# Optimization experiments

Measured on AMD Instinct MI355X. Metric: run time of the kernel, lower is better.

Reference implementation:

```python
import jax, jax.numpy as jnp
import numpy as np

EPS = 1.1920929e-07  # torch RMSNorm default eps = finfo(fp32).eps
NUM_HEADS = 8
UP_HEAD = 64
ROPE_HEAD = 32
TOP_K = 4
HIDDEN = 512
INTER = 256
DQ = 256
DKV = 128
N_EXPERTS = 16
B, S = 2, 2048


def _rmsnorm(x, w):
    return x * jax.lax.rsqrt(jnp.mean(x * x, axis=-1, keepdims=True) + EPS) * w


def _rope(x):
    # x: [B, h, S, D] with D = ROPE_HEAD; rotate-half RoPE, base 10000
    D = x.shape[-1]
    s = x.shape[-2]
    inv_freq = 1.0 / (10000.0 ** (jnp.arange(0, D, 2, dtype=jnp.float32) / D))
    freqs = jnp.outer(jnp.arange(s, dtype=jnp.float32), inv_freq)  # [S, D/2]
    emb = jnp.concatenate([freqs, freqs], axis=-1)  # [S, D]
    cos, sin = jnp.cos(emb), jnp.sin(emb)
    x1, x2 = x[..., : D // 2], x[..., D // 2:]
    rot = jnp.concatenate([-x2, x1], axis=-1)
    return x * cos + rot * sin


def _swiglu(x, wg, wu, wd):
    return (jax.nn.silu(x @ wg) * (x @ wu)) @ wd


def setup_inputs() -> dict:
    key = jax.random.key(0)
    ks = jax.random.split(key, 18)
    sd = 0.02
    inp = {
        "hidden_states": jax.random.normal(ks[0], (B, S, HIDDEN), jnp.float32),
        "w_in_norm": jnp.ones((HIDDEN,), jnp.float32),
        "w_dq": sd * jax.random.normal(ks[1], (HIDDEN, DQ), jnp.float32),
        "w_qnorm": jnp.ones((DQ,), jnp.float32),
        "w_uq": sd * jax.random.normal(ks[2], (DQ, NUM_HEADS * (UP_HEAD + ROPE_HEAD)), jnp.float32),
        "w_dkv": sd * jax.random.normal(ks[3], (HIDDEN, DKV + ROPE_HEAD), jnp.float32),
        "w_kvnorm": jnp.ones((DKV,), jnp.float32),
        "w_ukv": sd * jax.random.normal(ks[4], (DKV, NUM_HEADS * UP_HEAD * 2), jnp.float32),
        "w_o": sd * jax.random.normal(ks[5], (NUM_HEADS * UP_HEAD, HIDDEN), jnp.float32),
        "w_post_norm": jnp.ones((HIDDEN,), jnp.float32),
        "w_gate": sd * jax.random.normal(ks[6], (HIDDEN, N_EXPERTS), jnp.float32),
        "sh_wg": sd * jax.random.normal(ks[7], (HIDDEN, INTER), jnp.float32),
        "sh_wu": sd * jax.random.normal(ks[8], (HIDDEN, INTER), jnp.float32),
        "sh_wd": sd * jax.random.normal(ks[9], (INTER, HIDDEN), jnp.float32),
        "r_wg": sd * jax.random.normal(ks[10], (N_EXPERTS, HIDDEN, INTER), jnp.float32),
        "r_wu": sd * jax.random.normal(ks[11], (N_EXPERTS, HIDDEN, INTER), jnp.float32),
        "r_wd": sd * jax.random.normal(ks[12], (N_EXPERTS, INTER, HIDDEN), jnp.float32),
    }
    return inp


def reference(hidden_states, w_in_norm, w_dq, w_qnorm, w_uq, w_dkv, w_kvnorm,
              w_ukv, w_o, w_post_norm, w_gate, sh_wg, sh_wu, sh_wd,
              r_wg, r_wu, r_wd):
    b, s, h = hidden_states.shape
    # ---- MLA attention block ----
    residual = hidden_states
    x = _rmsnorm(hidden_states, w_in_norm)
    c_q = x @ w_dq                                             # [B,S,Dq]
    qcr = _rmsnorm(c_q, w_qnorm) @ w_uq                        # [B,S,nh*(uh+rh)]
    qcr = qcr.reshape(b, s, NUM_HEADS, UP_HEAD + ROPE_HEAD).transpose(0, 2, 1, 3)
    q_c, q_r = qcr[..., :UP_HEAD], qcr[..., UP_HEAD:]
    ckv_kr = x @ w_dkv                                         # [B,S,Dkv+rh]
    c_kv, k_r = ckv_kr[..., :DKV], ckv_kr[..., DKV:]
    k_r = k_r[:, None, :, :]                                   # [B,1,S,rh]
    kv = (_rmsnorm(c_kv, w_kvnorm) @ w_ukv).reshape(b, s, NUM_HEADS, 2 * UP_HEAD).transpose(0, 2, 1, 3)
    k_c, v = kv[..., :UP_HEAD], kv[..., UP_HEAD:]
    q = jnp.concatenate([q_c, _rope(q_r)], axis=-1)            # [B,nh,S,96]
    k = jnp.concatenate([k_c, jnp.broadcast_to(_rope(k_r), (b, NUM_HEADS, s, ROPE_HEAD))], axis=-1)
    scale = 1.0 / jnp.sqrt(jnp.float32(UP_HEAD + ROPE_HEAD))
    attn = jax.nn.softmax(jnp.einsum('bhqd,bhkd->bhqk', q, k) * scale, axis=-1)
    o = jnp.einsum('bhqk,bhkd->bhqd', attn, v).transpose(0, 2, 1, 3).reshape(b, s, NUM_HEADS * UP_HEAD)
    x = o @ w_o + residual
    # ---- MoE block ----
    residual = x
    x = _rmsnorm(x, w_post_norm)
    x2 = x.reshape(-1, h)                                      # [T,H]
    shared = _swiglu(x2, sh_wg, sh_wu, sh_wd)                  # [T,H]
    scores = jax.nn.sigmoid(x2 @ w_gate)                       # [T,E]
    tw, ti = jax.lax.top_k(scores, TOP_K)                      # [T,k]
    tw = tw / jnp.sum(tw, axis=-1, keepdims=True)
    # combine[t,e] = routing weight of expert e for token t (0 if not selected)
    combine = jnp.sum(jax.nn.one_hot(ti, N_EXPERTS, dtype=x2.dtype) * tw[..., None], axis=1)  # [T,E]
    g = jnp.einsum('th,ehi->tei', x2, r_wg)
    u = jnp.einsum('th,ehi->tei', x2, r_wu)
    y = jnp.einsum('tei,eih->teh', jax.nn.silu(g) * u, r_wd)   # per-expert SwiGLU outputs
    routed = jnp.einsum('teh,te->th', y, combine)
    return (shared + routed).reshape(b, s, h) + residual
```

## Files before the change

kernel.cpp:

```cpp
#include <hip/hip_runtime.h>
#include <hip/hip_bf16.h>
#include <math.h>

typedef float f32x4 __attribute__((ext_vector_type(4)));
typedef short s16x8 __attribute__((ext_vector_type(8)));

constexpr int Tt = 4096;
constexpr int NEn = 16;
constexpr float EPSf = 1.1920929e-07f;

__device__ __forceinline__ short f2b(float f) {
    union { __hip_bfloat16 h; short s; } u;
    u.h = __float2bfloat16(f);
    return u.s;
}
__device__ __forceinline__ float b2f(short s) {
    union { float f; unsigned u; } v;
    v.u = ((unsigned)(unsigned short)s) << 16;
    return v.f;
}

constexpr size_t alg(size_t x) { return (x + 15) & ~(size_t)15; }
constexpr size_t OFF_CQKV = 0;
constexpr size_t OFF_QCR  = alg(OFF_CQKV + (size_t)Tt * 416);
constexpr size_t OFF_KVB  = alg(OFF_QCR  + (size_t)Tt * 768);
constexpr size_t OFF_R2   = alg(OFF_KVB  + (size_t)Tt * 1024);
constexpr size_t OFF_TOKE = alg(OFF_R2   + (size_t)Tt * 512);
constexpr size_t OFF_TOKW = alg(OFF_TOKE + (size_t)Tt * 4);
constexpr size_t OFF_EWT  = alg(OFF_TOKW + (size_t)Tt * 4);
constexpr size_t OFF_ECNT = alg(OFF_EWT  + (size_t)NEn * Tt);
constexpr size_t OFF_ETOK = alg(OFF_ECNT + 64);
constexpr size_t OFF_PO   = 0;
constexpr size_t OFF_PL   = (size_t)16 * 2048 * 4 * 64 / 2;
constexpr size_t OFF_XNB   = alg(OFF_ETOK + (size_t)NEn * Tt);
constexpr size_t OFF_CQNB  = alg(OFF_XNB   + (size_t)Tt * 512 / 2);
constexpr size_t OFF_CKVNB = alg(OFF_CQNB  + (size_t)Tt * 256 / 2);
constexpr size_t OFF_QB    = alg(OFF_CKVNB + (size_t)Tt * 128 / 2);
constexpr size_t OFF_KB    = alg(OFF_QB    + (size_t)16 * 2048 * 96 / 2);
constexpr size_t OFF_VBT   = alg(OFF_KB    + (size_t)16 * 2048 * 96 / 2);
constexpr size_t OFF_XN2B  = alg(OFF_VBT   + (size_t)16 * 64 * 2048 / 2);
constexpr size_t OFF_GACT  = alg(OFF_XN2B  + (size_t)Tt * 512 / 2);
constexpr size_t OFF_EACT  = alg(OFF_GACT  + (size_t)Tt * 256 / 2);
constexpr size_t OFF_WQKVT = alg(OFF_EACT  + (size_t)16384 * 256 / 2);
constexpr size_t OFF_WUQT  = alg(OFF_WQKVT + (size_t)416 * 512 / 2);
constexpr size_t OFF_WUKVT = alg(OFF_WUQT  + (size_t)768 * 256 / 2);
constexpr size_t OFF_WOT   = alg(OFF_WUKVT + (size_t)1024 * 128 / 2);
constexpr size_t OFF_SHWGT = alg(OFF_WOT   + (size_t)512 * 512 / 2);
constexpr size_t OFF_SHWUT = alg(OFF_SHWGT + (size_t)256 * 512 / 2);
constexpr size_t OFF_SHWDT = alg(OFF_SHWUT + (size_t)256 * 512 / 2);
constexpr size_t OFF_RWGT  = alg(OFF_SHWDT + (size_t)512 * 256 / 2);
constexpr size_t OFF_RWUT  = alg(OFF_RWGT  + (size_t)16 * 256 * 512 / 2);
constexpr size_t OFF_RWDT  = alg(OFF_RWUT  + (size_t)16 * 256 * 512 / 2);

struct CvtTab {
    const float* src[11];
    short* dst[11];
    int K[11], N[11], end[11];
};
__global__ __launch_bounds__(256)
void k_cvt_all(CvtTab tab) {
    __shared__ float t[32][33];
    int bid = blockIdx.x;
    int i = 0;
    while (bid >= tab.end[i]) ++i;
    int tloc = bid - (i ? tab.end[i - 1] : 0);
    int K = tab.K[i], N = tab.N[i];
    int ntiles = N >> 5, perE = ntiles * (K >> 5);
    int e = tloc / perE, rem = tloc - e * perE;
    int k0 = (rem / ntiles) << 5, n0 = (rem % ntiles) << 5;
    size_t eo = (size_t)e * K * N;
    const float* src = tab.src[i];
    short* dst = tab.dst[i];
    int c = threadIdx.x & 31, r = threadIdx.x >> 5;
#pragma unroll
    for (int q = 0; q < 4; ++q)
        t[r + 8 * q][c] = src[eo + (size_t)(k0 + r + 8 * q) * N + n0 + c];
    __syncthreads();
#pragma unroll
    for (int q = 0; q < 4; ++q)
        dst[eo + (size_t)(n0 + r + 8 * q) * K + k0 + c] = f2b(t[c][r + 8 * q]);
}

__global__ void k_rms(const float* __restrict__ in, int inStride, const float* __restrict__ w,
                      short* __restrict__ outB, int outStride, int D) {
    int row = blockIdx.x, tid = threadIdx.x;
    __shared__ float xs[512];
    __shared__ float red[256];
    const float* ip = in + (size_t)row * inStride;
    float ss = 0.f;
    for (int i = tid; i < D; i += 256) { float v = ip[i]; xs[i] = v; ss += v * v; }
    red[tid] = ss; __syncthreads();
    for (int s = 128; s > 0; s >>= 1) { if (tid < s) red[tid] += red[tid + s]; __syncthreads(); }
    float sc = rsqrtf(red[0] / (float)D + EPSf);
    for (int i = tid; i < D; i += 256) outB[(size_t)row * outStride + i] = f2b(xs[i] * sc * w[i]);
}

__global__ void k_rms2(const float* __restrict__ cqkv, const float* __restrict__ wq, short* __restrict__ cqnb,
                       const float* __restrict__ wkv, short* __restrict__ ckvnb) {
    int row = blockIdx.x, tid = threadIdx.x;
    __shared__ float xs[256];
    __shared__ float red[256];
    const float* ip; const float* w; short* ob; int D, outStride, r;
    if (row < Tt) { r = row;      ip = cqkv + (size_t)r * 416;       w = wq;  ob = cqnb;  D = 256; outStride = 256; }
    else          { r = row - Tt; ip = cqkv + (size_t)r * 416 + 256; w = wkv; ob = ckvnb; D = 128; outStride = 128; }
    float ss = 0.f;
    for (int i = tid; i < D; i += 256) { float v = ip[i]; xs[i] = v; ss += v * v; }
    red[tid] = ss; __syncthreads();
    for (int s = 128; s > 0; s >>= 1) { if (tid < s) red[tid] += red[tid + s]; __syncthreads(); }
    float sc = rsqrtf(red[0] / (float)D + EPSf);
    for (int i = tid; i < D; i += 256) ob[(size_t)r * outStride + i] = f2b(xs[i] * sc * w[i]);
}

__global__ __launch_bounds__(256)
void k_rms_router(const float* __restrict__ r2, const float* __restrict__ wpost,
                  const float* __restrict__ wg,
                  short* __restrict__ xn2b, int4* __restrict__ toke, float4* __restrict__ tokw) {
    int t = blockIdx.x, tid = threadIdx.x;
    __shared__ float xs[512];
    __shared__ float red[256];
    __shared__ float part[16][17];
    __shared__ float sc[16];
    const float* ip = r2 + (size_t)t * 512;
    float ss = 0.f;
    for (int i = tid; i < 512; i += 256) { float v = ip[i]; xs[i] = v; ss += v * v; }
    red[tid] = ss; __syncthreads();
    for (int s = 128; s > 0; s >>= 1) { if (tid < s) red[tid] += red[tid + s]; __syncthreads(); }
    float scale = rsqrtf(red[0] / 512.f + EPSf);
    for (int i = tid; i < 512; i += 256) {
        float v = xs[i] * scale * wpost[i];
        xs[i] = v;
        xn2b[(size_t)t * 512 + i] = f2b(v);
    }
    __syncthreads();
    {
        int e = tid & 15, ch = tid >> 4;
        const float* wp = wg + (size_t)ch * 32 * 16 + e;
        float s = 0.f;
#pragma unroll 8
        for (int k = 0; k < 32; ++k) s = fmaf(xs[ch * 32 + k], wp[(size_t)k * 16], s);
        part[ch][e] = s;
    }
    __syncthreads();
    if (tid < 16) {
        float s = 0.f;
#pragma unroll
        for (int c = 0; c < 16; ++c) s += part[c][tid];
        sc[tid] = 1.f / (1.f + expf(-s));
    }
    __syncthreads();
    if (tid < 64) {
        int lane = tid, e = lane & 15;
        float scv = sc[e];
        unsigned sel = 0;
        float tw[4]; int ti[4];
#pragma unroll
        for (int kk = 0; kk < 4; ++kk) {
            float cand = ((sel >> e) & 1u) ? -1e30f : scv;
            float mx = cand;
            mx = fmaxf(mx, __shfl_xor(mx, 1));
            mx = fmaxf(mx, __shfl_xor(mx, 2));
            mx = fmaxf(mx, __shfl_xor(mx, 4));
            mx = fmaxf(mx, __shfl_xor(mx, 8));
            unsigned long long msk = __ballot(cand == mx);
            int bi = (__ffsll(msk) - 1) & 15;
            tw[kk] = mx; ti[kk] = bi;
            sel |= 1u << bi;
        }
        if (lane == 0) {
            float inv = 1.f / (tw[0] + tw[1] + tw[2] + tw[3]);
            toke[t] = make_int4(ti[0], ti[1], ti[2], ti[3]);
            tokw[t] = make_float4(tw[0] * inv, tw[1] * inv, tw[2] * inv, tw[3] * inv);
        }
    }
}

template <int EPI>
__global__ __launch_bounds__(512)
void k_mgemm(const short* __restrict__ A, const short* __restrict__ BT,
             void* __restrict__ Cv, const float* __restrict__ add, int N, int K) {
    __shared__ __align__(16) short As[64 * 64];
    __shared__ __align__(16) short Bs[64 * 64];
    int tid = threadIdx.x;
    int w = tid >> 6, l = tid & 63, g = l >> 4, li = l & 15;
    int wm = w >> 1, wn = w & 1;
    int m0 = blockIdx.y * 64, n0 = blockIdx.x * 64;
    f32x4 acc[2] = {};
    for (int k0 = 0; k0 < K; k0 += 64) {
        __syncthreads();
        {
            int row = tid >> 3, ch = tid & 7;
            *(int4*)&As[row * 64 + ((ch ^ (row & 7)) * 8)] =
                *(const int4*)(A + (size_t)(m0 + row) * K + k0 + 8 * ch);
            int4 v = {0, 0, 0, 0};
            if (n0 + row < N) v = *(const int4*)(BT + (size_t)(n0 + row) * K + k0 + 8 * ch);
            *(int4*)&Bs[row * 64 + ((ch ^ (row & 7)) * 8)] = v;
        }
        __syncthreads();
#pragma unroll
        for (int kc = 0; kc < 2; ++kc) {
            int row = wm * 16 + li;
            s16x8 af = *(const s16x8*)&As[row * 64 + (((4 * kc + g) ^ (li & 7)) * 8)];
#pragma unroll
            for (int nt = 0; nt < 2; ++nt) {
                int n = wn * 32 + nt * 16 + li;
                s16x8 bf = *(const s16x8*)&Bs[n * 64 + (((4 * kc + g) ^ (li & 7)) * 8)];
                acc[nt] = __builtin_amdgcn_mfma_f32_16x16x32_bf16(af, bf, acc[nt], 0, 0, 0);
            }
        }
    }
#pragma unroll
    for (int nt = 0; nt < 2; ++nt)
#pragma unroll
        for (int r = 0; r < 4; ++r) {
            int gm = m0 + wm * 16 + 4 * g + r;
            int gn = n0 + wn * 32 + nt * 16 + li;
            if (gn < N) {
                float v = acc[nt][r];
                if (EPI == 1) v += add[(size_t)gm * N + gn];
                if (EPI == 2) ((short*)Cv)[(size_t)gm * N + gn] = f2b(v);
                else          ((float*)Cv)[(size_t)gm * N + gn] = v;
            }
        }
}

__global__ __launch_bounds__(512)
void k_wo_gemm(const short* __restrict__ po, const float* __restrict__ pl,
               const short* __restrict__ BT, float* __restrict__ C,
               const float* __restrict__ add) {
    constexpr int N = 512, K = 512;
    __shared__ __align__(16) short As[64 * 64];
    __shared__ __align__(16) short Bs[64 * 64];
    int tid = threadIdx.x;
    int w = tid >> 6, l = tid & 63, g = l >> 4, li = l & 15;
    int wm = w >> 1, wn = w & 1;
    int m0 = blockIdx.y * 64, n0 = blockIdx.x * 64;
    int row = tid >> 3, ch = tid & 7;
    int t = m0 + row;
    int b = t >> 11, q = t & 2047;
    f32x4 acc[2] = {};
    for (int k0 = 0; k0 < K; k0 += 64) {
        int h = k0 >> 6;
        int bhq = (b * 8 + h) * 2048 + q;
        size_t pb = (size_t)bhq * 256 + 8 * ch;
        float4 l4 = *(const float4*)(pl + (size_t)bhq * 4);
        float inv = 1.f / (l4.x + l4.y + l4.z + l4.w);
        union { int4 v; short s[8]; } p0, p1, p2, p3, ov;
        p0.v = *(const int4*)(po + pb);
        p1.v = *(const int4*)(po + pb + 64);
        p2.v = *(const int4*)(po + pb + 128);
        p3.v = *(const int4*)(po + pb + 192);
#pragma unroll
        for (int i = 0; i < 8; ++i) {
            float os = b2f(p0.s[i]) + b2f(p1.s[i]) + b2f(p2.s[i]) + b2f(p3.s[i]);
            ov.s[i] = f2b(os * inv);
        }
        int4 bv = *(const int4*)(BT + (size_t)(n0 + row) * K + k0 + 8 * ch);
        __syncthreads();
        *(int4*)&As[row * 64 + ((ch ^ (row & 7)) * 8)] = ov.v;
        *(int4*)&Bs[row * 64 + ((ch ^ (row & 7)) * 8)] = bv;
        __syncthreads();
#pragma unroll
        for (int kc = 0; kc < 2; ++kc) {
            int rr = wm * 16 + li;
            s16x8 af = *(const s16x8*)&As[rr * 64 + (((4 * kc + g) ^ (li & 7)) * 8)];
#pragma unroll
            for (int nt = 0; nt < 2; ++nt) {
                int n = wn * 32 + nt * 16 + li;
                s16x8 bf = *(const s16x8*)&Bs[n * 64 + (((4 * kc + g) ^ (li & 7)) * 8)];
                acc[nt] = __builtin_amdgcn_mfma_f32_16x16x32_bf16(af, bf, acc[nt], 0, 0, 0);
            }
        }
    }
#pragma unroll
    for (int nt = 0; nt < 2; ++nt)
#pragma unroll
        for (int r = 0; r < 4; ++r) {
            int gm = m0 + wm * 16 + 4 * g + r;
            int gn = n0 + wn * 32 + nt * 16 + li;
            C[(size_t)gm * N + gn] = acc[nt][r] + add[(size_t)gm * N + gn];
        }
}

__global__ __launch_bounds__(512)
void k_shexp(const short* __restrict__ X, const short* __restrict__ WGt, const short* __restrict__ WUt,
             short* __restrict__ gact) {
    __shared__ __align__(16) short As[64 * 64];
    __shared__ __align__(16) short Bg[64 * 64];
    __shared__ __align__(16) short Bu[64 * 64];
    int tid = threadIdx.x;
    int w = tid >> 6, l = tid & 63, g = l >> 4, li = l & 15;
    int wm = w >> 1, wn = w & 1;
    int m0 = blockIdx.x * 64, n0 = blockIdx.y * 64;
    f32x4 ag[2] = {}, au[2] = {};
    for (int k0 = 0; k0 < 512; k0 += 64) {
        __syncthreads();
        {
            int row = tid >> 3, ch = tid & 7;
            *(int4*)&As[row * 64 + ((ch ^ (row & 7)) * 8)] =
                *(const int4*)(X + (size_t)(m0 + row) * 512 + k0 + 8 * ch);
            *(int4*)&Bg[row * 64 + ((ch ^ (row & 7)) * 8)] =
                *(const int4*)(WGt + (size_t)(n0 + row) * 512 + k0 + 8 * ch);
            *(int4*)&Bu[row * 64 + ((ch ^ (row & 7)) * 8)] =
                *(const int4*)(WUt + (size_t)(n0 + row) * 512 + k0 + 8 * ch);
        }
        __syncthreads();
#pragma unroll
        for (int kc = 0; kc < 2; ++kc) {
            int row = wm * 16 + li;
            s16x8 af = *(const s16x8*)&As[row * 64 + (((4 * kc + g) ^ (li & 7)) * 8)];
#pragma unroll
            for (int nt = 0; nt < 2; ++nt) {
                int n = wn * 32 + nt * 16 + li;
                s16x8 bg = *(const s16x8*)&Bg[n * 64 + (((4 * kc + g) ^ (li & 7)) * 8)];
                s16x8 bu = *(const s16x8*)&Bu[n * 64 + (((4 * kc + g) ^ (li & 7)) * 8)];
                ag[nt] = __builtin_amdgcn_mfma_f32_16x16x32_bf16(af, bg, ag[nt], 0, 0, 0);
                au[nt] = __builtin_amdgcn_mfma_f32_16x16x32_bf16(af, bu, au[nt], 0, 0, 0);
            }
        }
    }
#pragma unroll
    for (int nt = 0; nt < 2; ++nt)
#pragma unroll
        for (int r = 0; r < 4; ++r) {
            int gm = m0 + wm * 16 + 4 * g + r;
            int gn = n0 + wn * 32 + nt * 16 + li;
            float gv = ag[nt][r], uv = au[nt][r];
            gact[(size_t)gm * 256 + gn] = f2b(gv / (1.f + __expf(-gv)) * uv);
        }
}

__global__ void k_build_qkv(const short* __restrict__ qcrb, const short* __restrict__ kvbb,
                            const float* __restrict__ cqkv,
                            short* __restrict__ qb, short* __restrict__ kb, short* __restrict__ vbt) {
    const float scale = 0.14724389f;
    int gid = blockIdx.x * 256 + threadIdx.x;
    const int NQ = 16 * 2048 * 96;
    if (gid < NQ) {
        int d = gid % 96;
        int rs = gid / 96;
        int srow = rs & 2047;
        int bh = rs >> 11;
        int b = bh >> 3, h = bh & 7;
        int t = b * 2048 + srow;
        const short* src = qcrb + (size_t)t * 768 + h * 96;
        float val;
        if (d < 64) {
            val = b2f(src[d]);
        } else {
            int d2 = d - 64;
            int fi = d2 & 15;
            float ang = (float)srow * __expf(-((float)(2 * fi) / 32.f) * 9.210340371976184f);
            float s, c; __sincosf(ang, &s, &c);
            float x = b2f(src[64 + d2]);
            float r = (d2 < 16) ? -b2f(src[64 + d2 + 16]) : b2f(src[64 + d2 - 16]);
            val = x * c + r * s;
        }
        qb[gid] = f2b(val * scale);
    } else if (gid < 2 * NQ) {
        int g2 = gid - NQ;
        int d = g2 % 96;
        int rs = g2 / 96;
        int srow = rs & 2047;
        int bh = rs >> 11;
        int b = bh >> 3, h = bh & 7;
        int t = b * 2048 + srow;
        if (d < 64) {
            kb[g2] = kvbb[(size_t)t * 1024 + h * 128 + d];
        } else {
            int d2 = d - 64;
            int fi = d2 & 15;
            float ang = (float)srow * __expf(-((float)(2 * fi) / 32.f) * 9.210340371976184f);
            float s, c; __sincosf(ang, &s, &c);
            float x = cqkv[(size_t)t * 416 + 384 + d2];
            float r = (d2 < 16) ? -cqkv[(size_t)t * 416 + 384 + d2 + 16]
                                :  cqkv[(size_t)t * 416 + 384 + d2 - 16];
            kb[g2] = f2b(x * c + r * s);
        }
    } else {
        int g2 = gid - 2 * NQ;
        int key = g2 & 2047;
        int dim = (g2 >> 11) & 63;
        int bh = g2 >> 17;
        int b = bh >> 3, h = bh & 7;
        vbt[g2] = kvbb[(size_t)(b * 2048 + key) * 1024 + h * 128 + 64 + dim];
    }
}

__global__ __launch_bounds__(256)
void k_attn(const short* __restrict__ qb, const short* __restrict__ kb,
            const short* __restrict__ vbt, short* __restrict__ po, float* __restrict__ pl) {
    __shared__ __align__(16) short Ks[64 * 100];
    __shared__ __align__(16) short Vs[80 * 64];
    int tid = threadIdx.x;
    int w = tid >> 6, l = tid & 63, g = l >> 4, li = l & 15;
    int blk = blockIdx.x;
    int bh = blk >> 6, rem = blk & 63;
    int qt = rem >> 2, ks = rem & 3;
    int qc0 = qt * 128 + w * 32;

    {
        const short one = 0x3F80;
        for (int i = tid; i < 16 * 64; i += 256)
            Vs[64 * 64 + i] = (i < 64) ? one : (short)0;
    }

    s16x8 qf[2][3];
#pragma unroll
    for (int j = 0; j < 2; ++j) {
        const short* qp = qb + (size_t)(bh * 2048 + qc0 + j * 16 + li) * 96;
#pragma unroll
        for (int c = 0; c < 3; ++c) qf[j][c] = *(const s16x8*)(qp + 32 * c + 8 * g);
    }

    f32x4 o[2][5] = {};
    const short* kbase = kb + (size_t)bh * 2048 * 96;
    const short* vbase = vbt + (size_t)bh * 64 * 2048;

    for (int t = 0; t < 8; ++t) {
        int koff = ks * 512 + t * 64;
        __syncthreads();
#pragma unroll
        for (int p = 0; p < 3; ++p) {
            int flat = p * 256 + tid;
            int key = flat / 12, u = flat % 12;
            *(int4*)&Ks[key * 100 + 8 * u] = *(const int4*)(kbase + (size_t)(koff + key) * 96 + 8 * u);
        }
#pragma unroll
        for (int p = 0; p < 2; ++p) {
            int flat = p * 256 + tid;
            int dim = flat >> 3, kc8 = flat & 7;
            int4 v = *(const int4*)(vbase + (size_t)dim * 2048 + koff + 8 * kc8);
            int sw = dim & 15;
            *(int2*)&Vs[dim * 64 + (((2 * kc8) ^ sw) * 4)]     = make_int2(v.x, v.y);
            *(int2*)&Vs[dim * 64 + (((2 * kc8 + 1) ^ sw) * 4)] = make_int2(v.z, v.w);
        }
        __syncthreads();

        f32x4 s[2][4];
#pragma unroll
        for (int kt = 0; kt < 4; ++kt) {
            f32x4 a0 = {}, a1 = {};
#pragma unroll
            for (int c = 0; c < 3; ++c) {
                s16x8 kf = *(const s16x8*)&Ks[(kt * 16 + li) * 100 + 32 * c + 8 * g];
                a0 = __builtin_amdgcn_mfma_f32_16x16x32_bf16(kf, qf[0][c], a0, 0, 0, 0);
                a1 = __builtin_amdgcn_mfma_f32_16x16x32_bf16(kf, qf[1][c], a1, 0, 0, 0);
            }
            s[0][kt] = a0; s[1][kt] = a1;
        }
#pragma unroll
        for (int j = 0; j < 2; ++j)
#pragma unroll
            for (int kt = 0; kt < 4; ++kt)
#pragma unroll
                for (int r = 0; r < 4; ++r) s[j][kt][r] = exp2f(s[j][kt][r]);
        s16x8 pf[2][2];
#pragma unroll
        for (int j = 0; j < 2; ++j)
#pragma unroll
            for (int kc = 0; kc < 2; ++kc) {
                s16x8 tt;
#pragma unroll
                for (int r = 0; r < 4; ++r) { tt[r] = f2b(s[j][2 * kc][r]); tt[4 + r] = f2b(s[j][2 * kc + 1][r]); }
                pf[j][kc] = tt;
            }
#pragma unroll
        for (int dt = 0; dt < 5; ++dt) {
            int dim = dt * 16 + li;
#pragma unroll
            for (int kc = 0; kc < 2; ++kc) {
                int2 a0 = *(const int2*)&Vs[dim * 64 + (((8 * kc + g) ^ li) * 4)];
                int2 a1 = *(const int2*)&Vs[dim * 64 + (((8 * kc + 4 + g) ^ li) * 4)];
                union { s16x8 v; int i[4]; } vf;
                vf.i[0] = a0.x; vf.i[1] = a0.y; vf.i[2] = a1.x; vf.i[3] = a1.y;
                o[0][dt] = __builtin_amdgcn_mfma_f32_16x16x32_bf16(vf.v, pf[0][kc], o[0][dt], 0, 0, 0);
                o[1][dt] = __builtin_amdgcn_mfma_f32_16x16x32_bf16(vf.v, pf[1][kc], o[1][dt], 0, 0, 0);
            }
        }
    }
#pragma unroll
    for (int j = 0; j < 2; ++j) {
        int qcol = qc0 + j * 16 + li;
        size_t qbase = ((size_t)(bh * 2048 + qcol) * 4 + ks) * 64;
#pragma unroll
        for (int dt = 0; dt < 4; ++dt)
#pragma unroll
            for (int r = 0; r < 4; ++r)
                po[qbase + dt * 16 + 4 * g + r] = f2b(o[j][dt][r]);
        if (g == 0) pl[(size_t)(bh * 2048 + qcol) * 4 + ks] = o[j][4][0];
    }
}

__global__ __launch_bounds__(256)
void k_scatter(const int4* __restrict__ toke, const float4* __restrict__ tokw,
               float* __restrict__ ewt, int* __restrict__ ecnt, int* __restrict__ etok) {
    __shared__ int lcnt[16];
    __shared__ int lbase[16];
    int tid = threadIdx.x;
    int t = blockIdx.x * 256 + tid;
    if (tid < 16) lcnt[tid] = 0;
    __syncthreads();
    int4 e4 = toke[t];
    float4 w4 = tokw[t];
    int es[4] = { e4.x, e4.y, e4.z, e4.w };
    float wv[4] = { w4.x, w4.y, w4.z, w4.w };
    int ls[4];
#pragma unroll
    for (int kk = 0; kk < 4; ++kk) ls[kk] = atomicAdd(&lcnt[es[kk]], 1);
    __syncthreads();
    if (tid < 16) lbase[tid] = atomicAdd(&ecnt[tid], lcnt[tid]);
    __syncthreads();
#pragma unroll
    for (int kk = 0; kk < 4; ++kk) {
        int slot = lbase[es[kk]] + ls[kk];
        etok[es[kk] * 4096 + slot] = t * 4 + kk;
        ewt[es[kk] * 4096 + slot] = wv[kk];
    }
}

__global__ __launch_bounds__(512)
void k_moe1m(const short* __restrict__ X, const short* __restrict__ WGt, const short* __restrict__ WUt,
             const int* __restrict__ ecnt, const int* __restrict__ etok, short* __restrict__ eact) {
    __shared__ int ecs[16];
    __shared__ __align__(16) short As[128 * 64];
    __shared__ __align__(16) short Bg[64 * 64];
    __shared__ __align__(16) short Bu[64 * 64];
    __shared__ int toks[128];
    int tid = threadIdx.x;
    if (tid < 16) ecs[tid] = ecnt[tid];
    __syncthreads();
    int bid = blockIdx.x, e = 0;
    for (; e < 16; ++e) { int n = (ecs[e] + 127) >> 7; if (bid < n) break; bid -= n; }
    if (e >= 16) return;
    int base = bid << 7;
    int rows = min(128, ecs[e] - base);
    int n0 = blockIdx.y * 64;
    if (tid < 128) toks[tid] = (tid < rows) ? etok[e * 4096 + base + tid] : -1;
    __syncthreads();
    int w = tid >> 6, l = tid & 63, g = l >> 4, li = l & 15;
    int wm = w >> 1, wn = w & 1;
    const short* wgp = WGt + (size_t)e * 256 * 512;
    const short* wup = WUt + (size_t)e * 256 * 512;
    f32x4 ag[2][2] = {}, au[2][2] = {};
    for (int k0 = 0; k0 < 512; k0 += 64) {
        __syncthreads();
#pragma unroll
        for (int p = 0; p < 2; ++p) {
            int flat = p * 512 + tid;
            int row = flat >> 3, ch = flat & 7;
            int tk = toks[row];
            int4 v = {0, 0, 0, 0};
            if (tk >= 0) v = *(const int4*)(X + (size_t)(tk >> 2) * 512 + k0 + 8 * ch);
            *(int4*)&As[row * 64 + ((ch ^ (row & 7)) * 8)] = v;
        }
        {
            int n = tid >> 3, ch = tid & 7;
            *(int4*)&Bg[n * 64 + ((ch ^ (n & 7)) * 8)] = *(const int4*)(wgp + (size_t)(n0 + n) * 512 + k0 + 8 * ch);
            *(int4*)&Bu[n * 64 + ((ch ^ (n & 7)) * 8)] = *(const int4*)(wup + (size_t)(n0 + n) * 512 + k0 + 8 * ch);
        }
        __syncthreads();
#pragma unroll
        for (int kc = 0; kc < 2; ++kc) {
            s16x8 af[2], bg[2], bu[2];
#pragma unroll
            for (int mt = 0; mt < 2; ++mt) {
                int row = wm * 32 + mt * 16 + li;
                af[mt] = *(const s16x8*)&As[row * 64 + (((4 * kc + g) ^ (li & 7)) * 8)];
            }
#pragma unroll
            for (int nt = 0; nt < 2; ++nt) {
                int n = wn * 32 + nt * 16 + li;
                bg[nt] = *(const s16x8*)&Bg[n * 64 + (((4 * kc + g) ^ (li & 7)) * 8)];
                bu[nt] = *(const s16x8*)&Bu[n * 64 + (((4 * kc + g) ^ (li & 7)) * 8)];
            }
#pragma unroll
            for (int mt = 0; mt < 2; ++mt)
#pragma unroll
                for (int nt = 0; nt < 2; ++nt) {
                    ag[mt][nt] = __builtin_amdgcn_mfma_f32_16x16x32_bf16(af[mt], bg[nt], ag[mt][nt], 0, 0, 0);
                    au[mt][nt] = __builtin_amdgcn_mfma_f32_16x16x32_bf16(af[mt], bu[nt], au[mt][nt], 0, 0, 0);
                }
        }
    }
#pragma unroll
    for (int mt = 0; mt < 2; ++mt)
#pragma unroll
        for (int nt = 0; nt < 2; ++nt)
#pragma unroll
            for (int r = 0; r < 4; ++r) {
                int local = wm * 32 + mt * 16 + 4 * g + r;
                if (local < rows) {
                    int entry = toks[local];
                    int gn = n0 + wn * 32 + nt * 16 + li;
                    float gv = ag[mt][nt][r], uv = au[mt][nt][r];
                    eact[(size_t)entry * 256 + gn] = f2b(gv / (1.f + __expf(-gv)) * uv);
                }
            }
}

__global__ __launch_bounds__(512)
void k_moe2m(const short* __restrict__ EA, const short* __restrict__ WDt,
             const int* __restrict__ ecnt, const int* __restrict__ etok,
             const float* __restrict__ ewt, float* __restrict__ oacc) {
    __shared__ int ecs[16];
    __shared__ __align__(16) short As[128 * 64];
    __shared__ __align__(16) short Bs[64 * 64];
    __shared__ int toks[128];
    __shared__ float wts[128];
    int tid = threadIdx.x;
    if (tid < 16) ecs[tid] = ecnt[tid];
    __syncthreads();
    int bid = blockIdx.x, e = 0;
    for (; e < 16; ++e) { int n = (ecs[e] + 127) >> 7; if (bid < n) break; bid -= n; }
    if (e >= 16) return;
    int base = bid << 7;
    int rows = min(128, ecs[e] - base);
    int n0 = blockIdx.y * 64;
    if (tid < 128) {
        toks[tid] = (tid < rows) ? etok[e * 4096 + base + tid] : -1;
        wts[tid]  = (tid < rows) ? ewt[e * 4096 + base + tid] : 0.f;
    }
    __syncthreads();
    int w = tid >> 6, l = tid & 63, g = l >> 4, li = l & 15;
    int wm = w >> 1, wn = w & 1;
    const short* wdp = WDt + (size_t)e * 512 * 256;
    f32x4 acc[2][2] = {};
    for (int k0 = 0; k0 < 256; k0 += 64) {
        __syncthreads();
#pragma unroll
        for (int p = 0; p < 2; ++p) {
            int flat = p * 512 + tid;
            int row = flat >> 3, ch = flat & 7;
            int tk = toks[row];
            int4 v = {0, 0, 0, 0};
            if (tk >= 0) v = *(const int4*)(EA + (size_t)tk * 256 + k0 + 8 * ch);
            *(int4*)&As[row * 64 + ((ch ^ (row & 7)) * 8)] = v;
        }
        {
            int n = tid >> 3, ch = tid & 7;
            *(int4*)&Bs[n * 64 + ((ch ^ (n & 7)) * 8)] = *(const int4*)(wdp + (size_t)(n0 + n) * 256 + k0 + 8 * ch);
        }
        __syncthreads();
#pragma unroll
        for (int kc = 0; kc < 2; ++kc) {
            s16x8 af[2], bf[2];
#pragma unroll
            for (int mt = 0; mt < 2; ++mt) {
                int row = wm * 32 + mt * 16 + li;
                af[mt] = *(const s16x8*)&As[row * 64 + (((4 * kc + g) ^ (li & 7)) * 8)];
            }
#pragma unroll
            for (int nt = 0; nt < 2; ++nt) {
                int n = wn * 32 + nt * 16 + li;
                bf[nt] = *(const s16x8*)&Bs[n * 64 + (((4 * kc + g) ^ (li & 7)) * 8)];
            }
#pragma unroll
            for (int mt = 0; mt < 2; ++mt)
#pragma unroll
                for (int nt = 0; nt < 2; ++nt)
                    acc[mt][nt] = __builtin_amdgcn_mfma_f32_16x16x32_bf16(af[mt], bf[nt], acc[mt][nt], 0, 0, 0);
        }
    }
#pragma unroll
    for (int mt = 0; mt < 2; ++mt)
#pragma unroll
        for (int nt = 0; nt < 2; ++nt)
#pragma unroll
            for (int r = 0; r < 4; ++r) {
                int local = wm * 32 + mt * 16 + 4 * g + r;
                if (local < rows) {
                    int tok = toks[local] >> 2;
                    int gn = n0 + wn * 32 + nt * 16 + li;
                    atomicAdd(&oacc[(size_t)tok * 512 + gn], acc[mt][nt][r] * wts[local]);
                }
            }
}

extern "C" void kernel_launch(void* const* d_in, const int* in_sizes, int n_in,
                              void* d_out, int out_size, void* d_ws, size_t ws_size,
                              hipStream_t stream) {
    const float* hs       = (const float*)d_in[0];
    const float* w_innorm = (const float*)d_in[1];
    const float* w_dq     = (const float*)d_in[2];
    const float* w_qnorm  = (const float*)d_in[3];
    const float* w_uq     = (const float*)d_in[4];
    const float* w_dkv    = (const float*)d_in[5];
    const float* w_kvnorm = (const float*)d_in[6];
    const float* w_ukv    = (const float*)d_in[7];
    const float* w_o      = (const float*)d_in[8];
    const float* w_post   = (const float*)d_in[9];
    const float* w_gate   = (const float*)d_in[10];
    const float* sh_wg    = (const float*)d_in[11];
    const float* sh_wu    = (const float*)d_in[12];
    const float* sh_wd    = (const float*)d_in[13];
    const float* r_wg     = (const float*)d_in[14];
    const float* r_wu     = (const float*)d_in[15];
    const float* r_wd     = (const float*)d_in[16];

    float* ws   = (float*)d_ws;
    float* cqkv = ws + OFF_CQKV;
    short* qcrb = (short*)(ws + OFF_QCR);
    short* kvbb = (short*)(ws + OFF_KVB);
    float* r2   = ws + OFF_R2;
    short* po   = (short*)(ws + OFF_PO);
    float* pl   = ws + OFF_PL;
    int4*  toke = (int4*)(ws + OFF_TOKE);
    float4* tokw = (float4*)(ws + OFF_TOKW);
    float* ewt  = ws + OFF_EWT;
    int*   ecnt = (int*)(ws + OFF_ECNT);
    int*   etok = (int*)(ws + OFF_ETOK);
    short* xnb   = (short*)(ws + OFF_XNB);
    short* cqnb  = (short*)(ws + OFF_CQNB);
    short* ckvnb = (short*)(ws + OFF_CKVNB);
    short* qb    = (short*)(ws + OFF_QB);
    short* kb    = (short*)(ws + OFF_KB);
    short* vbt   = (short*)(ws + OFF_VBT);
    short* xn2b  = (short*)(ws + OFF_XN2B);
    short* gact  = (short*)(ws + OFF_GACT);
    short* eact  = (short*)(ws + OFF_EACT);
    short* wqkvT = (short*)(ws + OFF_WQKVT);
    short* wuqT  = (short*)(ws + OFF_WUQT);
    short* wukvT = (short*)(ws + OFF_WUKVT);
    short* woT   = (short*)(ws + OFF_WOT);
    short* shwgT = (short*)(ws + OFF_SHWGT);
    short* shwuT = (short*)(ws + OFF_SHWUT);
    short* shwdT = (short*)(ws + OFF_SHWDT);
    short* rwgT  = (short*)(ws + OFF_RWGT);
    short* rwuT  = (short*)(ws + OFF_RWUT);
    short* rwdT  = (short*)(ws + OFF_RWDT);

    float* outF = (float*)d_out;

    CvtTab tab;
    const float* srcs[11] = { w_dq, w_dkv, w_uq, w_ukv, w_o, sh_wg, sh_wu, sh_wd, r_wg, r_wu, r_wd };
    short* dsts[11] = { wqkvT, wqkvT + (size_t)256 * 512, wuqT, wukvT, woT, shwgT, shwuT, shwdT, rwgT, rwuT, rwdT };
    int Ks_[11] = { 512, 512, 256, 128, 512, 512, 512, 256, 512, 512, 256 };
    int Ns_[11] = { 256, 160, 768, 1024, 512, 256, 256, 512, 256, 256, 512 };
    int Es_[11] = { 1, 1, 1, 1, 1, 1, 1, 1, 16, 16, 16 };
    int cum = 0;
    for (int i = 0; i < 11; ++i) {
        tab.src[i] = srcs[i]; tab.dst[i] = dsts[i];
        tab.K[i] = Ks_[i]; tab.N[i] = Ns_[i];
        cum += Es_[i] * (Ks_[i] >> 5) * (Ns_[i] >> 5);
        tab.end[i] = cum;
    }
    k_cvt_all<<<cum, 256, 0, stream>>>(tab);

    k_rms<<<Tt, 256, 0, stream>>>(hs, 512, w_innorm, xnb, 512, 512);
    k_mgemm<0><<<dim3(7, 64), 512, 0, stream>>>(xnb, wqkvT, (void*)cqkv, nullptr, 416, 512);
    k_rms2<<<2 * Tt, 256, 0, stream>>>(cqkv, w_qnorm, cqnb, w_kvnorm, ckvnb);
    k_mgemm<2><<<dim3(12, 64), 512, 0, stream>>>(cqnb, wuqT, (void*)qcrb, nullptr, 768, 256);
    k_mgemm<2><<<dim3(16, 64), 512, 0, stream>>>(ckvnb, wukvT, (void*)kvbb, nullptr, 1024, 128);
    k_build_qkv<<<(2 * 16 * 2048 * 96 + 16 * 64 * 2048) / 256, 256, 0, stream>>>(qcrb, kvbb, cqkv, qb, kb, vbt);
    k_attn<<<1024, 256, 0, stream>>>(qb, kb, vbt, po, pl);
    k_wo_gemm<<<dim3(8, 64), 512, 0, stream>>>(po, pl, woT, r2, hs);
    k_rms_router<<<Tt, 256, 0, stream>>>(r2, w_post, w_gate, xn2b, toke, tokw);
    k_shexp<<<dim3(64, 4), 512, 0, stream>>>(xn2b, shwgT, shwuT, gact);
    k_mgemm<1><<<dim3(8, 64), 512, 0, stream>>>(gact, shwdT, (void*)outF, r2, 512, 256);
    hipMemsetAsync(ecnt, 0, NEn * sizeof(int), stream);
    k_scatter<<<16, 256, 0, stream>>>(toke, tokw, ewt, ecnt, etok);
    k_moe1m<<<dim3(144, 4), 512, 0, stream>>>(xn2b, rwgT, rwuT, ecnt, etok, eact);
    k_moe2m<<<dim3(144, 8), 512, 0, stream>>>(eact, rwdT, ecnt, etok, ewt, outF);
}
```

Baseline: 229.1 us.

## Double attention key tile, vectorize output stores, fold ecnt reset into rms

The attention kernel now stages 128 keys per iteration instead of 64. That halves the number of barrier-separated load phases while keeping the same MFMA compute split into two 64-key halves. Partial-output stores are packed into 8-byte writes instead of scalar shorts. The separate hipMemsetAsync for the expert counters is removed, and the first block of the input RMSNorm kernel zeroes them instead, saving one stream operation. The larger LDS footprint may reduce occupancy of the attention kernel.

```diff
diff --git a/kernel.cpp b/kernel.cpp
--- a/kernel.cpp
+++ b/kernel.cpp
@@ -82,8 +82,9 @@
 }
 
 __global__ void k_rms(const float* __restrict__ in, int inStride, const float* __restrict__ w,
-                      short* __restrict__ outB, int outStride, int D) {
+                      short* __restrict__ outB, int outStride, int D, int* __restrict__ ecnt) {
     int row = blockIdx.x, tid = threadIdx.x;
+    if (row == 0 && tid < 16) ecnt[tid] = 0;
     __shared__ float xs[512];
     __shared__ float red[256];
     const float* ip = in + (size_t)row * inStride;
@@ -389,8 +390,8 @@
 __global__ __launch_bounds__(256)
 void k_attn(const short* __restrict__ qb, const short* __restrict__ kb,
             const short* __restrict__ vbt, short* __restrict__ po, float* __restrict__ pl) {
-    __shared__ __align__(16) short Ks[64 * 100];
-    __shared__ __align__(16) short Vs[80 * 64];
+    __shared__ __align__(16) short Ks[128 * 100];
+    __shared__ __align__(16) short Vs[80 * 128];
     int tid = threadIdx.x;
     int w = tid >> 6, l = tid & 63, g = l >> 4, li = l & 15;
     int blk = blockIdx.x;
@@ -400,8 +401,8 @@
 
     {
         const short one = 0x3F80;
-        for (int i = tid; i < 16 * 64; i += 256)
-            Vs[64 * 64 + i] = (i < 64) ? one : (short)0;
+        for (int i = tid; i < 16 * 128; i += 256)
+            Vs[64 * 128 + i] = (i < 128) ? one : (short)0;
     }
 
     s16x8 qf[2][3];
@@ -416,65 +417,69 @@
     const short* kbase = kb + (size_t)bh * 2048 * 96;
     const short* vbase = vbt + (size_t)bh * 64 * 2048;
 
-    for (int t = 0; t < 8; ++t) {
-        int koff = ks * 512 + t * 64;
-        __syncthreads();
-#pragma unroll
-        for (int p = 0; p < 3; ++p) {
+    for (int t = 0; t < 4; ++t) {
+        int koff = ks * 512 + t * 128;
+        __syncthreads();
+#pragma unroll
+        for (int p = 0; p < 6; ++p) {
             int flat = p * 256 + tid;
             int key = flat / 12, u = flat % 12;
             *(int4*)&Ks[key * 100 + 8 * u] = *(const int4*)(kbase + (size_t)(koff + key) * 96 + 8 * u);
         }
 #pragma unroll
-        for (int p = 0; p < 2; ++p) {
+        for (int p = 0; p < 4; ++p) {
             int flat = p * 256 + tid;
-            int dim = flat >> 3, kc8 = flat & 7;
+            int dim = flat >> 4, kc8 = flat & 15;
             int4 v = *(const int4*)(vbase + (size_t)dim * 2048 + koff + 8 * kc8);
             int sw = dim & 15;
-            *(int2*)&Vs[dim * 64 + (((2 * kc8) ^ sw) * 4)]     = make_int2(v.x, v.y);
-            *(int2*)&Vs[dim * 64 + (((2 * kc8 + 1) ^ sw) * 4)] = make_int2(v.z, v.w);
-        }
-        __syncthreads();
-
-        f32x4 s[2][4];
-#pragma unroll
-        for (int kt = 0; kt < 4; ++kt) {
-            f32x4 a0 = {}, a1 = {};
-#pragma unroll
-            for (int c = 0; c < 3; ++c) {
-                s16x8 kf = *(const s16x8*)&Ks[(kt * 16 + li) * 100 + 32 * c + 8 * g];
-                a0 = __builtin_amdgcn_mfma_f32_16x16x32_bf16(kf, qf[0][c], a0, 0, 0, 0);
-                a1 = __builtin_amdgcn_mfma_f32_16x16x32_bf16(kf, qf[1][c], a1, 0, 0, 0);
-            }
-            s[0][kt] = a0; s[1][kt] = a1;
-        }
-#pragma unroll
-        for (int j = 0; j < 2; ++j)
-#pragma unroll
-            for (int kt = 0; kt < 4; ++kt)
-#pragma unroll
-                for (int r = 0; r < 4; ++r) s[j][kt][r] = exp2f(s[j][kt][r]);
-        s16x8 pf[2][2];
-#pragma unroll
-        for (int j = 0; j < 2; ++j)
-#pragma unroll
-            for (int kc = 0; kc < 2; ++kc) {
-                s16x8 tt;
-#pragma unroll
-                for (int r = 0; r < 4; ++r) { tt[r] = f2b(s[j][2 * kc][r]); tt[4 + r] = f2b(s[j][2 * kc + 1][r]); }
-                pf[j][kc] = tt;
-            }
-#pragma unroll
-        for (int dt = 0; dt < 5; ++dt) {
-            int dim = dt * 16 + li;
-#pragma unroll
-            for (int kc = 0; kc < 2; ++kc) {
-                int2 a0 = *(const int2*)&Vs[dim * 64 + (((8 * kc + g) ^ li) * 4)];
-                int2 a1 = *(const int2*)&Vs[dim * 64 + (((8 * kc + 4 + g) ^ li) * 4)];
-                union { s16x8 v; int i[4]; } vf;
-                vf.i[0] = a0.x; vf.i[1] = a0.y; vf.i[2] = a1.x; vf.i[3] = a1.y;
-                o[0][dt] = __builtin_amdgcn_mfma_f32_16x16x32_bf16(vf.v, pf[0][kc], o[0][dt], 0, 0, 0);
-                o[1][dt] = __builtin_amdgcn_mfma_f32_16x16x32_bf16(vf.v, pf[1][kc], o[1][dt], 0, 0, 0);
+            *(int2*)&Vs[dim * 128 + (((2 * kc8) ^ sw) * 4)]     = make_int2(v.x, v.y);
+            *(int2*)&Vs[dim * 128 + (((2 * kc8 + 1) ^ sw) * 4)] = make_int2(v.z, v.w);
+        }
+        __syncthreads();
+
+#pragma unroll
+        for (int h = 0; h < 2; ++h) {
+            f32x4 s[2][4];
+#pragma unroll
+            for (int kt = 0; kt < 4; ++kt) {
+                f32x4 a0 = {}, a1 = {};
+#pragma unroll
+                for (int c = 0; c < 3; ++c) {
+                    s16x8 kf = *(const s16x8*)&Ks[(64 * h + kt * 16 + li) * 100 + 32 * c + 8 * g];
+                    a0 = __builtin_amdgcn_mfma_f32_16x16x32_bf16(kf, qf[0][c], a0, 0, 0, 0);
+                    a1 = __builtin_amdgcn_mfma_f32_16x16x32_bf16(kf, qf[1][c], a1, 0, 0, 0);
+                }
+                s[0][kt] = a0; s[1][kt] = a1;
+            }
+#pragma unroll
+            for (int j = 0; j < 2; ++j)
+#pragma unroll
+                for (int kt = 0; kt < 4; ++kt)
+#pragma unroll
+                    for (int r = 0; r < 4; ++r) s[j][kt][r] = exp2f(s[j][kt][r]);
+            s16x8 pf[2][2];
+#pragma unroll
+            for (int j = 0; j < 2; ++j)
+#pragma unroll
+                for (int kcl = 0; kcl < 2; ++kcl) {
+                    s16x8 tt;
+#pragma unroll
+                    for (int r = 0; r < 4; ++r) { tt[r] = f2b(s[j][2 * kcl][r]); tt[4 + r] = f2b(s[j][2 * kcl + 1][r]); }
+                    pf[j][kcl] = tt;
+                }
+#pragma unroll
+            for (int dt = 0; dt < 5; ++dt) {
+                int dim = dt * 16 + li;
+#pragma unroll
+                for (int kcl = 0; kcl < 2; ++kcl) {
+                    int kc = 2 * h + kcl;
+                    int2 a0 = *(const int2*)&Vs[dim * 128 + (((8 * kc + g) ^ li) * 4)];
+                    int2 a1 = *(const int2*)&Vs[dim * 128 + (((8 * kc + 4 + g) ^ li) * 4)];
+                    union { s16x8 v; int i[4]; } vf;
+                    vf.i[0] = a0.x; vf.i[1] = a0.y; vf.i[2] = a1.x; vf.i[3] = a1.y;
+                    o[0][dt] = __builtin_amdgcn_mfma_f32_16x16x32_bf16(vf.v, pf[0][kcl], o[0][dt], 0, 0, 0);
+                    o[1][dt] = __builtin_amdgcn_mfma_f32_16x16x32_bf16(vf.v, pf[1][kcl], o[1][dt], 0, 0, 0);
+                }
             }
         }
     }
@@ -483,10 +488,12 @@
         int qcol = qc0 + j * 16 + li;
         size_t qbase = ((size_t)(bh * 2048 + qcol) * 4 + ks) * 64;
 #pragma unroll
-        for (int dt = 0; dt < 4; ++dt)
-#pragma unroll
-            for (int r = 0; r < 4; ++r)
-                po[qbase + dt * 16 + 4 * g + r] = f2b(o[j][dt][r]);
+        for (int dt = 0; dt < 4; ++dt) {
+            union { short s[4]; int2 v; } pk;
+#pragma unroll
+            for (int r = 0; r < 4; ++r) pk.s[r] = f2b(o[j][dt][r]);
+            *(int2*)(po + qbase + dt * 16 + 4 * g) = pk.v;
+        }
         if (g == 0) pl[(size_t)(bh * 2048 + qcol) * 4 + ks] = o[j][4][0];
     }
 }
@@ -746,7 +753,7 @@
     }
     k_cvt_all<<<cum, 256, 0, stream>>>(tab);
 
-    k_rms<<<Tt, 256, 0, stream>>>(hs, 512, w_innorm, xnb, 512, 512);
+    k_rms<<<Tt, 256, 0, stream>>>(hs, 512, w_innorm, xnb, 512, 512, ecnt);
     k_mgemm<0><<<dim3(7, 64), 512, 0, stream>>>(xnb, wqkvT, (void*)cqkv, nullptr, 416, 512);
     k_rms2<<<2 * Tt, 256, 0, stream>>>(cqkv, w_qnorm, cqnb, w_kvnorm, ckvnb);
     k_mgemm<2><<<dim3(12, 64), 512, 0, stream>>>(cqnb, wuqT, (void*)qcrb, nullptr, 768, 256);
@@ -757,7 +764,6 @@
     k_rms_router<<<Tt, 256, 0, stream>>>(r2, w_post, w_gate, xn2b, toke, tokw);
     k_shexp<<<dim3(64, 4), 512, 0, stream>>>(xn2b, shwgT, shwuT, gact);
     k_mgemm<1><<<dim3(8, 64), 512, 0, stream>>>(gact, shwdT, (void*)outF, r2, 512, 256);
-    hipMemsetAsync(ecnt, 0, NEn * sizeof(int), stream);
     k_scatter<<<16, 256, 0, stream>>>(toke, tokw, ewt, ecnt, etok);
     k_moe1m<<<dim3(144, 4), 512, 0, stream>>>(xn2b, rwgT, rwuT, ecnt, etok, eact);
     k_moe2m<<<dim3(144, 8), 512, 0, stream>>>(eact, rwdT, ecnt, etok, ewt, outF);
```

After: 241.8 us. +5.6%, slower.
